# Kernel optimization log

Measured on AMD Instinct MI355X. Metric: run time of the kernel, lower is better.

## Reference

```python
import jax, jax.numpy as jnp
import numpy as np

DIM = 256
HEAD_DIM = 64
NH = DIM // HEAD_DIM
PS = 2  # fine patch size
EPS = 1e-5


def _conv(x, w, b, stride, pad):
    y = jax.lax.conv_general_dilated(x, w, (stride, stride), ((pad, pad), (pad, pad)),
                                     dimension_numbers=('NCHW', 'OIHW', 'NCHW'))
    return y + b[None, :, None, None]


def _bn(x, g, b, m, v):
    s = g * jax.lax.rsqrt(v + EPS)
    return x * s[None, :, None, None] + (b - m * s)[None, :, None, None]


def setup_inputs() -> dict:
    key = jax.random.key(0)
    ks = jax.random.split(key, 24)
    C = DIM
    d = {}
    d['x'] = jax.random.normal(ks[0], (8, C, 64, 64), jnp.float32)
    # Downsample conv (C->C, k=4, s=2, p=1), torch OIHW layout
    d['w_down'] = jax.random.normal(ks[1], (C, C, 4, 4), jnp.float32) * 0.02
    d['b_down'] = jax.random.normal(ks[2], (C,), jnp.float32) * 0.02
    # coarse to_qkv Linear(64 -> 192), stored as [in, out]
    d['w_qkv_c'] = jax.random.normal(ks[3], (HEAD_DIM, 3 * HEAD_DIM), jnp.float32) * 0.05
    d['b_qkv_c'] = jax.random.normal(ks[4], (3 * HEAD_DIM,), jnp.float32) * 0.02
    # Upsample ConvTranspose2d (torch [in, out, kH, kW] layout)
    d['w_up'] = jax.random.normal(ks[5], (C, C, 4, 4), jnp.float32) * 0.02
    d['b_up'] = jax.random.normal(ks[6], (C,), jnp.float32) * 0.02
    # fine to_qkv Linear(64 -> 192)
    d['w_qkv_f'] = jax.random.normal(ks[7], (HEAD_DIM, 3 * HEAD_DIM), jnp.float32) * 0.05
    d['b_qkv_f'] = jax.random.normal(ks[8], (3 * HEAD_DIM,), jnp.float32) * 0.02
    # DWConv: depthwise 3x3 (groups=C) -> BN -> relu6 -> pointwise 1x1 -> BN -> relu6
    d['w_dw'] = jax.random.normal(ks[9], (C, 1, 3, 3), jnp.float32) * 0.1
    d['bn_dw_g'] = jax.random.uniform(ks[10], (C,), jnp.float32) * 0.5 + 0.75
    d['bn_dw_b'] = jax.random.normal(ks[11], (C,), jnp.float32) * 0.1
    d['bn_dw_m'] = jax.random.normal(ks[12], (C,), jnp.float32) * 0.1
    d['bn_dw_v'] = jax.random.uniform(ks[13], (C,), jnp.float32) + 0.5
    d['w_pw'] = jax.random.normal(ks[14], (C, C, 1, 1), jnp.float32) * 0.05
    d['bn_pw_g'] = jax.random.uniform(ks[15], (C,), jnp.float32) * 0.5 + 0.75
    d['bn_pw_b'] = jax.random.normal(ks[16], (C,), jnp.float32) * 0.1
    d['bn_pw_m'] = jax.random.normal(ks[17], (C,), jnp.float32) * 0.1
    d['bn_pw_v'] = jax.random.uniform(ks[18], (C,), jnp.float32) + 0.5
    return d


def reference(x, w_down, b_down, w_qkv_c, b_qkv_c, w_up, b_up, w_qkv_f, b_qkv_f,
              w_dw, bn_dw_g, bn_dw_b, bn_dw_m, bn_dw_v,
              w_pw, bn_pw_g, bn_pw_b, bn_pw_m, bn_pw_v):
    B, C, H, W = x.shape
    nh, hd = C // HEAD_DIM, HEAD_DIM
    scale = hd ** -0.5

    # ---- CoarseSelfAttention ----
    xd = _conv(x, w_down, b_down, 2, 1)           # [B,C,h,w]
    h, w = xd.shape[2], xd.shape[3]
    P = h * w
    tok = xd.reshape(B, nh, hd, P).transpose(0, 1, 3, 2)   # [B,nh,P,hd]
    q, k, v = jnp.split(tok @ w_qkv_c + b_qkv_c, 3, axis=-1)
    attn = jax.nn.softmax(jnp.einsum('bhqd,bhkd->bhqk', q, k) * scale, axis=-1)
    coarse_score = attn.sum(axis=-2)               # [B,nh,P]
    kf = max(1, P // 4)
    top_k = jax.lax.top_k(coarse_score, kf)[1]     # [B,nh,kf]
    out = jnp.einsum('bhqk,bhkd->bhqd', attn, v)
    out = out.transpose(0, 1, 3, 2).reshape(B, C, h, w)
    # ConvTranspose2d(k=4,s=2,p=1) as lhs-dilated conv with flipped/transposed kernel
    wt = jnp.flip(w_up, (2, 3)).transpose(1, 0, 2, 3)
    coarse = jax.lax.conv_general_dilated(out, wt, (1, 1), ((2, 2), (2, 2)),
                                          lhs_dilation=(2, 2),
                                          dimension_numbers=('NCHW', 'OIHW', 'NCHW'))
    coarse = coarse + b_up[None, :, None, None]
    # F.interpolate to (H,W) is identity here: upsample exactly restores HxW

    # ---- TopkSelfAttention ----
    ph, pw = H // PS, W // PS                      # ph*pw == P
    xh = coarse.reshape(B, nh, hd, ph, PS, pw, PS)
    patches = xh.transpose(0, 1, 2, 3, 5, 4, 6).reshape(B, nh, hd, ph * pw, PS, PS)
    idx = jnp.broadcast_to(top_k[:, :, None, :, None, None], (B, nh, hd, kf, PS, PS))
    sel = jnp.take_along_axis(patches, idx, axis=3)        # [B,nh,hd,kf,PS,PS]
    tokf = sel.reshape(B, nh, hd, kf, PS * PS).transpose(0, 1, 3, 4, 2)
    tokf = tokf.reshape(B, nh, kf * PS * PS, hd)
    qf, kk, vf = jnp.split(tokf @ w_qkv_f + b_qkv_f, 3, axis=-1)
    attnf = jax.nn.softmax(jnp.einsum('bhqd,bhkd->bhqk', qf, kk) * scale, axis=-1)
    outf = jnp.einsum('bhqk,bhkd->bhqd', attnf, vf)
    outf = outf.reshape(B, nh, kf, PS * PS, hd).transpose(0, 1, 2, 4, 3)
    outf = outf.reshape(B, nh, kf, hd, PS, PS)     # [B,nh,kf,hd,PS,PS]
    # scatter selected patches back into zeros (topk indices are unique per b,h)
    res = jnp.zeros((B, nh, ph * pw, hd, PS, PS), x.dtype)
    bi = jnp.arange(B)[:, None, None]
    hi = jnp.arange(nh)[None, :, None]
    res = res.at[bi, hi, top_k].set(outf)
    res = res.transpose(0, 1, 3, 2, 4, 5).reshape(B, nh, hd, ph, pw, PS, PS)
    region = res.transpose(0, 1, 2, 3, 5, 4, 6).reshape(B, C, H, W)

    y = coarse + region

    # ---- DWConv feed-forward ----
    yd = jax.lax.conv_general_dilated(y, w_dw, (1, 1), ((1, 1), (1, 1)),
                                      feature_group_count=C,
                                      dimension_numbers=('NCHW', 'OIHW', 'NCHW'))
    yd = jnp.clip(_bn(yd, bn_dw_g, bn_dw_b, bn_dw_m, bn_dw_v), 0.0, 6.0)
    yp = jax.lax.conv_general_dilated(yd, w_pw, (1, 1), ((0, 0), (0, 0)),
                                      dimension_numbers=('NCHW', 'OIHW', 'NCHW'))
    yp = jnp.clip(_bn(yp, bn_pw_g, bn_pw_b, bn_pw_m, bn_pw_v), 0.0, 6.0)
    return yp
```

## Files before the change

kernel.cpp:

```cpp
#include <hip/hip_runtime.h>
#include <cstdint>
#include <cstddef>


#define EPS_ 1e-5f

typedef short bf16x8_t __attribute__((ext_vector_type(8)));
typedef float f32x4_t __attribute__((ext_vector_type(4)));
#define MFMA16(a, b, c) __builtin_amdgcn_mfma_f32_16x16x32_bf16(a, b, c, 0, 0, 0)

__device__ __forceinline__ void cvt1(float f, unsigned short& h, unsigned short& l) {
  unsigned u = __float_as_uint(f);
  unsigned r = u + 0x7FFFu + ((u >> 16) & 1u);
  h = (unsigned short)(r >> 16);
  float lo = f - __uint_as_float(r & 0xFFFF0000u);
  l = (unsigned short)(__float_as_uint(lo) >> 16);
}
__device__ __forceinline__ unsigned cvtpack(float f) {
  unsigned short h, l;
  cvt1(f, h, l);
  return (unsigned)h | ((unsigned)l << 16);
}
__device__ __forceinline__ void cvt2(float f0, float f1, unsigned& hpack, unsigned& lpack) {
  unsigned u0 = __float_as_uint(f0), u1 = __float_as_uint(f1);
  unsigned r0 = u0 + 0x7FFFu + ((u0 >> 16) & 1u);
  unsigned r1 = u1 + 0x7FFFu + ((u1 >> 16) & 1u);
  hpack = (r0 >> 16) | (r1 & 0xFFFF0000u);
  float l0 = f0 - __uint_as_float(r0 & 0xFFFF0000u);
  float l1 = f1 - __uint_as_float(r1 & 0xFFFF0000u);
  lpack = (__float_as_uint(l0) >> 16) | (__float_as_uint(l1) & 0xFFFF0000u);
}
__device__ __forceinline__ unsigned pk_h(unsigned a, unsigned b) {
  return (a & 0xFFFFu) | (b << 16);
}
__device__ __forceinline__ unsigned pk_l(unsigned a, unsigned b) {
  return (a >> 16) | (b & 0xFFFF0000u);
}

__global__ __launch_bounds__(256) void k_pad_x(
    const float* __restrict__ x, unsigned* __restrict__ xphl) {
  const int plane = blockIdx.x;
  const float* src = x + (size_t)plane * 4096;
  unsigned* dst = xphl + (size_t)plane * 4488;
  for (int e = threadIdx.x; e < 4356; e += 256) {
    int r = e / 66, cc = e - r * 66;
    float v = 0.f;
    if (r >= 1 && r <= 64 && cc >= 1 && cc <= 64) v = src[(r - 1) * 64 + (cc - 1)];
    dst[r * 68 + cc] = cvtpack(v);
  }
}

__global__ __launch_bounds__(256) void k_cvt_wdown(
    const float* __restrict__ w, unsigned short* __restrict__ wh,
    unsigned short* __restrict__ wl) {
  int e = blockIdx.x * 256 + threadIdx.x;
  cvt1(w[e], wh[e], wl[e]);
}

__global__ __launch_bounds__(256) void k_cvt_wqkv(
    const float* __restrict__ wq, unsigned short* __restrict__ wh,
    unsigned short* __restrict__ wl) {
  int e = blockIdx.x * 256 + threadIdx.x;
  int col = e >> 6, d = e & 63;
  float f = wq[d * 192 + col];
  if (col < 64) f *= 0.125f;
  cvt1(f, wh[e], wl[e]);
}

__global__ __launch_bounds__(256) void k_cvt_wup(
    const float* __restrict__ w_up, unsigned short* __restrict__ wth,
    unsigned short* __restrict__ wtl) {
  int e = blockIdx.x * 256 + threadIdx.x;
  int kp = e & 1023, oc = (e >> 10) & 255, c = e >> 18;
  int tap = kp >> 8, ic = kp & 255;
  int tk = tap >> 1, txi = tap & 1;
  int ry = c >> 1, rx = c & 1;
  int ky = (1 - ry) + 2 * tk, kx = (1 - rx) + 2 * txi;
  cvt1(w_up[((size_t)(ic * 256 + oc) * 4 + ky) * 4 + kx], wth[e], wtl[e]);
}

__global__ __launch_bounds__(256) void k_cvt_wpw(
    const float* __restrict__ w, unsigned short* __restrict__ wh,
    unsigned short* __restrict__ wl) {
  int e = blockIdx.x * 256 + threadIdx.x;
  cvt1(w[e], wh[e], wl[e]);
}

__device__ __forceinline__ void mfma_chunk(
    const unsigned short (*Ah)[72], const unsigned short (*Al)[72],
    const unsigned short (*Bh)[72], const unsigned short (*Bl)[72],
    f32x4_t (&acc)[4], int wm, int lane) {
  const int l16 = lane & 15, quad = lane >> 4;
#pragma unroll
  for (int ks = 0; ks < 2; ++ks) {
    int ko = ks * 32 + quad * 8;
    bf16x8_t ah = *(const bf16x8_t*)&Ah[wm + l16][ko];
    bf16x8_t al = *(const bf16x8_t*)&Al[wm + l16][ko];
#pragma unroll
    for (int nt = 0; nt < 4; ++nt) {
      bf16x8_t bh = *(const bf16x8_t*)&Bh[nt * 16 + l16][ko];
      bf16x8_t bl = *(const bf16x8_t*)&Bl[nt * 16 + l16][ko];
      acc[nt] = MFMA16(ah, bh, acc[nt]);
      acc[nt] = MFMA16(ah, bl, acc[nt]);
      acc[nt] = MFMA16(al, bh, acc[nt]);
    }
  }
}

__global__ __launch_bounds__(256) void k_conv_down_mfma(
    const unsigned* __restrict__ xphl, const unsigned short* __restrict__ wdh,
    const unsigned short* __restrict__ wdl, const float* __restrict__ bias,
    unsigned* __restrict__ xdhl) {
  __shared__ unsigned short Ah[64][72], Al[64][72], Bh[64][72], Bl[64][72];
  const int t = threadIdx.x;
  const int pix0 = blockIdx.x * 64, oc0 = blockIdx.y * 64;
  const int bimg = pix0 >> 10, pos = pix0 & 1023;
  const int pl = t & 63, icg = t >> 6;
  const int rem = (pix0 + pl) & 1023;
  const int oy = rem >> 5, ox = rem & 31;
  const unsigned* xb = xphl + ((size_t)bimg * 256 + icg) * 4488 + (oy * 2) * 68 + ox * 2;
  const int wave = t >> 6, lane = t & 63, l16 = lane & 15, quad = lane >> 4;
  const int ar = t >> 3, akc = (t & 7) * 8;
  f32x4_t acc[4] = {};
  for (int kb = 0; kb < 4096; kb += 64) {
    bf16x8_t a0h = *(const bf16x8_t*)(wdh + (size_t)(oc0 + ar) * 4096 + kb + akc);
    bf16x8_t a0l = *(const bf16x8_t*)(wdl + (size_t)(oc0 + ar) * 4096 + kb + akc);
    bf16x8_t a1h = *(const bf16x8_t*)(wdh + (size_t)(oc0 + 32 + ar) * 4096 + kb + akc);
    bf16x8_t a1l = *(const bf16x8_t*)(wdl + (size_t)(oc0 + 32 + ar) * 4096 + kb + akc);
    unsigned hA[8], lA[8];
#pragma unroll
    for (int r = 0; r < 4; ++r) {
      uint2 u01 = *(const uint2*)(xb + r * 68);
      uint2 u23 = *(const uint2*)(xb + r * 68 + 2);
      hA[2 * r] = pk_h(u01.x, u01.y); hA[2 * r + 1] = pk_h(u23.x, u23.y);
      lA[2 * r] = pk_l(u01.x, u01.y); lA[2 * r + 1] = pk_l(u23.x, u23.y);
    }
    __syncthreads();
    *(bf16x8_t*)&Ah[ar][akc] = a0h;      *(bf16x8_t*)&Al[ar][akc] = a0l;
    *(bf16x8_t*)&Ah[ar + 32][akc] = a1h; *(bf16x8_t*)&Al[ar + 32][akc] = a1l;
    *(uint4*)&Bh[pl][icg * 16] = make_uint4(hA[0], hA[1], hA[2], hA[3]);
    *(uint4*)&Bh[pl][icg * 16 + 8] = make_uint4(hA[4], hA[5], hA[6], hA[7]);
    *(uint4*)&Bl[pl][icg * 16] = make_uint4(lA[0], lA[1], lA[2], lA[3]);
    *(uint4*)&Bl[pl][icg * 16 + 8] = make_uint4(lA[4], lA[5], lA[6], lA[7]);
    __syncthreads();
    mfma_chunk(Ah, Al, Bh, Bl, acc, wave * 16, lane);
    xb += 4 * 4488;
  }
#pragma unroll
  for (int r = 0; r < 4; ++r) {
    int oc = oc0 + wave * 16 + quad * 4 + r;
    float bv = bias[oc];
#pragma unroll
    for (int nt = 0; nt < 4; ++nt)
      xdhl[((size_t)(bimg * 256 + oc)) * 1024 + pos + nt * 16 + l16] =
          cvtpack(acc[nt][r] + bv);
  }
}

template <int MODE>
__global__ __launch_bounds__(256) void k_qkv_mfma(
    const unsigned* __restrict__ srcp, const float* __restrict__ srcf,
    const unsigned short* __restrict__ wh, const unsigned short* __restrict__ wl,
    const float* __restrict__ bq, const int* __restrict__ topk,
    unsigned short* __restrict__ qh, unsigned short* __restrict__ ql,
    unsigned short* __restrict__ kh, unsigned short* __restrict__ kl,
    unsigned short* __restrict__ vth, unsigned short* __restrict__ vtl) {
  __shared__ unsigned short Ah[64][72], Al[64][72];
  const int t = threadIdx.x;
  const int tok0 = blockIdx.x * 64;
  const int pair = blockIdx.y;
  const int b = pair >> 2, h = pair & 3;
  const int tokl = t & 63, dg = t >> 6;
  unsigned hp[8], lp[8];
  if (MODE == 0) {
    const unsigned* base = srcp + ((size_t)(b * 256 + h * 64 + dg * 16)) * 1024 + tok0 + tokl;
    unsigned u[16];
#pragma unroll
    for (int j = 0; j < 16; ++j) u[j] = base[(size_t)j * 1024];
#pragma unroll
    for (int j = 0; j < 8; ++j) {
      hp[j] = pk_h(u[2 * j], u[2 * j + 1]);
      lp[j] = pk_l(u[2 * j], u[2 * j + 1]);
    }
  } else {
    int tok = tok0 + tokl;
    int pp = topk[pair * 256 + (tok >> 2)];
    int py = (tok >> 1) & 1, px = tok & 1;
    int ry = (pp >> 5) * 2 + py, rx = (pp & 31) * 2 + px;
    const float* base = srcf + ((size_t)(b * 256 + h * 64 + dg * 16)) * 4096 + ry * 64 + rx;
    float fv[16];
#pragma unroll
    for (int j = 0; j < 16; ++j) fv[j] = base[(size_t)j * 4096];
#pragma unroll
    for (int j = 0; j < 8; ++j) cvt2(fv[2 * j], fv[2 * j + 1], hp[j], lp[j]);
  }
  *(uint4*)&Ah[tokl][dg * 16] = make_uint4(hp[0], hp[1], hp[2], hp[3]);
  *(uint4*)&Ah[tokl][dg * 16 + 8] = make_uint4(hp[4], hp[5], hp[6], hp[7]);
  *(uint4*)&Al[tokl][dg * 16] = make_uint4(lp[0], lp[1], lp[2], lp[3]);
  *(uint4*)&Al[tokl][dg * 16 + 8] = make_uint4(lp[4], lp[5], lp[6], lp[7]);
  __syncthreads();
  const int wave = t >> 6, lane = t & 63, l16 = lane & 15, quad = lane >> 4;
  f32x4_t acc[4][3] = {};
#pragma unroll
  for (int ks = 0; ks < 2; ++ks) {
    int ko = ks * 32 + quad * 8;
    bf16x8_t bh0[3], bl0[3];
#pragma unroll
    for (int nt = 0; nt < 3; ++nt) {
      int col = wave * 48 + nt * 16 + l16;
      bh0[nt] = *(const bf16x8_t*)(wh + col * 64 + ko);
      bl0[nt] = *(const bf16x8_t*)(wl + col * 64 + ko);
    }
#pragma unroll
    for (int mt = 0; mt < 4; ++mt) {
      bf16x8_t ah = *(const bf16x8_t*)&Ah[mt * 16 + l16][ko];
      bf16x8_t al = *(const bf16x8_t*)&Al[mt * 16 + l16][ko];
#pragma unroll
      for (int nt = 0; nt < 3; ++nt) {
        acc[mt][nt] = MFMA16(ah, bh0[nt], acc[mt][nt]);
        acc[mt][nt] = MFMA16(ah, bl0[nt], acc[mt][nt]);
        acc[mt][nt] = MFMA16(al, bh0[nt], acc[mt][nt]);
      }
    }
  }
#pragma unroll
  for (int nt = 0; nt < 3; ++nt) {
    int col = wave * 48 + nt * 16 + l16;
    float bqv = bq[col];
    if (col < 64) bqv *= 0.125f;
#pragma unroll
    for (int mt = 0; mt < 4; ++mt) {
#pragma unroll
      for (int r = 0; r < 4; ++r) {
        int tok = tok0 + mt * 16 + quad * 4 + r;
        float val = acc[mt][nt][r] + bqv;
        unsigned short hh, ll;
        cvt1(val, hh, ll);
        if (col < 64) {
          size_t o = ((size_t)pair * 1024 + tok) * 64 + col;
          qh[o] = hh; ql[o] = ll;
        } else if (col < 128) {
          size_t o = ((size_t)pair * 1024 + tok) * 64 + (col - 64);
          kh[o] = hh; kl[o] = ll;
        } else {
          size_t o = ((size_t)pair * 64 + (col - 128)) * 1024 + tok;
          vth[o] = hh; vtl[o] = ll;
        }
      }
    }
  }
}

template <int COARSE>
__global__ __launch_bounds__(256) void k_attn(
    const unsigned short* __restrict__ qh, const unsigned short* __restrict__ ql,
    const unsigned short* __restrict__ kh, const unsigned short* __restrict__ kl,
    const unsigned short* __restrict__ vth, const unsigned short* __restrict__ vtl,
    float* __restrict__ score, unsigned* __restrict__ outc,
    float* __restrict__ outf) {
  __shared__ __align__(16) unsigned short Qb[2][64][72];
  __shared__ __align__(16) unsigned short Kb[2][64][72];
  __shared__ __align__(16) unsigned short Pb[2][64][72];
  __shared__ float mlW[4][2][64];
  __shared__ float mC[64], lC[64];
  __shared__ float colsum[1024];
  const int t = threadIdx.x;
  const int q0 = blockIdx.x * 64;
  const int pair = blockIdx.y;
  const int wave = t >> 6, lane = t & 63;
  const int l16 = lane & 15, quad = lane >> 4;
  const int wm = wave * 16;
  const int sr = t >> 3, skc = (t & 7) * 8;

  const size_t qbase = ((size_t)pair * 1024 + q0) * 64;
#pragma unroll
  for (int i = 0; i < 2; ++i) {
    int r = sr + i * 32;
    *(bf16x8_t*)&Qb[0][r][skc] = *(const bf16x8_t*)(qh + qbase + (size_t)r * 64 + skc);
    *(bf16x8_t*)&Qb[1][r][skc] = *(const bf16x8_t*)(ql + qbase + (size_t)r * 64 + skc);
  }
  if (COARSE) {
#pragma unroll
    for (int i = 0; i < 4; ++i) colsum[t + i * 256] = 0.f;
  }

  const size_t kmbase = (size_t)pair * 1024 * 64;
  const size_t vbase = (size_t)pair * 64 * 1024;

  float mrun[4] = {-1e30f, -1e30f, -1e30f, -1e30f};
  float lrun[4] = {0.f, 0.f, 0.f, 0.f};
  for (int kb = 0; kb < 1024; kb += 64) {
    __syncthreads();
#pragma unroll
    for (int i = 0; i < 2; ++i) {
      int r = sr + i * 32;
      *(bf16x8_t*)&Kb[0][r][skc] = *(const bf16x8_t*)(kh + kmbase + (size_t)(kb + r) * 64 + skc);
      *(bf16x8_t*)&Kb[1][r][skc] = *(const bf16x8_t*)(kl + kmbase + (size_t)(kb + r) * 64 + skc);
    }
    __syncthreads();
    f32x4_t acc[4] = {};
    mfma_chunk(Kb[0], Kb[1], Qb[0], Qb[1], acc, wm, lane);
#pragma unroll
    for (int nt = 0; nt < 4; ++nt) {
      float m0 = fmaxf(fmaxf(acc[nt][0], acc[nt][1]), fmaxf(acc[nt][2], acc[nt][3]));
      m0 = fmaxf(m0, __shfl_xor(m0, 16));
      m0 = fmaxf(m0, __shfl_xor(m0, 32));
      float mn = fmaxf(mrun[nt], m0);
      float s0 = __expf(acc[nt][0] - mn) + __expf(acc[nt][1] - mn) +
                 __expf(acc[nt][2] - mn) + __expf(acc[nt][3] - mn);
      s0 += __shfl_xor(s0, 16);
      s0 += __shfl_xor(s0, 32);
      lrun[nt] = lrun[nt] * __expf(mrun[nt] - mn) + s0;
      mrun[nt] = mn;
    }
  }
  __syncthreads();
  if (quad == 0) {
#pragma unroll
    for (int nt = 0; nt < 4; ++nt) {
      mlW[wave][0][nt * 16 + l16] = mrun[nt];
      mlW[wave][1][nt * 16 + l16] = lrun[nt];
    }
  }
  __syncthreads();
  if (t < 64) {
    float m0 = mlW[0][0][t], m1 = mlW[1][0][t], m2 = mlW[2][0][t], m3 = mlW[3][0][t];
    float mm = fmaxf(fmaxf(m0, m1), fmaxf(m2, m3));
    float ll = mlW[0][1][t] * __expf(m0 - mm) + mlW[1][1][t] * __expf(m1 - mm) +
               mlW[2][1][t] * __expf(m2 - mm) + mlW[3][1][t] * __expf(m3 - mm);
    mC[t] = mm;
    lC[t] = 1.0f / ll;
  }
  __syncthreads();
  float mq[4], il[4];
#pragma unroll
  for (int nt = 0; nt < 4; ++nt) {
    mq[nt] = mC[nt * 16 + l16];
    il[nt] = lC[nt * 16 + l16];
  }

  f32x4_t accO[4] = {};
  for (int kb = 0; kb < 1024; kb += 64) {
    __syncthreads();
#pragma unroll
    for (int i = 0; i < 2; ++i) {
      int r = sr + i * 32;
      *(bf16x8_t*)&Kb[0][r][skc] = *(const bf16x8_t*)(kh + kmbase + (size_t)(kb + r) * 64 + skc);
      *(bf16x8_t*)&Kb[1][r][skc] = *(const bf16x8_t*)(kl + kmbase + (size_t)(kb + r) * 64 + skc);
    }
    __syncthreads();
    f32x4_t acc[4] = {};
    mfma_chunk(Kb[0], Kb[1], Qb[0], Qb[1], acc, wm, lane);
    float P[4][4];
#pragma unroll
    for (int nt = 0; nt < 4; ++nt)
#pragma unroll
      for (int r = 0; r < 4; ++r) P[nt][r] = __expf(acc[nt][r] - mq[nt]) * il[nt];
    if (COARSE) {
#pragma unroll
      for (int r = 0; r < 4; ++r) {
        float cs = P[0][r] + P[1][r] + P[2][r] + P[3][r];
        cs += __shfl_xor(cs, 1);
        cs += __shfl_xor(cs, 2);
        cs += __shfl_xor(cs, 4);
        cs += __shfl_xor(cs, 8);
        if (l16 == 0) colsum[kb + wm + quad * 4 + r] += cs;
      }
    }
    __syncthreads();
#pragma unroll
    for (int nt = 0; nt < 4; ++nt) {
      unsigned h01, l01, h23, l23;
      cvt2(P[nt][0], P[nt][1], h01, l01);
      cvt2(P[nt][2], P[nt][3], h23, l23);
      *(uint2*)&Pb[0][nt * 16 + l16][wm + quad * 4] = make_uint2(h01, h23);
      *(uint2*)&Pb[1][nt * 16 + l16][wm + quad * 4] = make_uint2(l01, l23);
    }
#pragma unroll
    for (int i = 0; i < 2; ++i) {
      int r = sr + i * 32;
      *(bf16x8_t*)&Kb[0][r][skc] = *(const bf16x8_t*)(vth + vbase + (size_t)r * 1024 + kb + skc);
      *(bf16x8_t*)&Kb[1][r][skc] = *(const bf16x8_t*)(vtl + vbase + (size_t)r * 1024 + kb + skc);
    }
    __syncthreads();
    mfma_chunk(Pb[0], Pb[1], Kb[0], Kb[1], accO, wm, lane);
  }
  __syncthreads();

  if (COARSE) {
#pragma unroll
    for (int i = 0; i < 4; ++i)
      atomicAdd(&score[pair * 1024 + t + i * 256], colsum[t + i * 256]);
    float (*Tr)[68] = reinterpret_cast<float(*)[68]>(&Pb[0][0][0]);
#pragma unroll
    for (int nt = 0; nt < 4; ++nt)
#pragma unroll
      for (int r = 0; r < 4; ++r)
        Tr[nt * 16 + l16][wm + quad * 4 + r] = accO[nt][r];
    __syncthreads();
    const int b = pair >> 2, h = pair & 3;
#pragma unroll
    for (int i = 0; i < 16; ++i) {
      int e = t + i * 256;
      int d = e >> 6, ql_ = e & 63;
      int pix = q0 + ql_;
      int iy = (pix >> 5) + 1, ix = (pix & 31) + 1;
      outc[((size_t)(b * 256 + h * 64 + d)) * 1156 + iy * 34 + ix] = cvtpack(Tr[d][ql_]);
    }
  } else {
#pragma unroll
    for (int nt = 0; nt < 4; ++nt)
#pragma unroll
      for (int r = 0; r < 4; ++r) {
        int qm = q0 + wm + quad * 4 + r;
        outf[((size_t)pair * 1024 + qm) * 64 + nt * 16 + l16] = accO[nt][r];
      }
  }
}

__global__ __launch_bounds__(256) void k_topk(
    const float* __restrict__ score, int* __restrict__ idx) {
  __shared__ unsigned long long key[1024];
  const int pair = blockIdx.x;
  const int t = threadIdx.x;
#pragma unroll
  for (int j = 0; j < 4; ++j) {
    int i = t + j * 256;
    unsigned u = __float_as_uint(score[pair * 1024 + i]);
    u = u ^ ((u & 0x80000000u) ? 0xFFFFFFFFu : 0x80000000u);
    u = ~u;
    key[i] = ((unsigned long long)u << 32) | (unsigned)i;
  }
  __syncthreads();
  for (int k = 2; k <= 1024; k <<= 1) {
    for (int j = k >> 1; j > 0; j >>= 1) {
      for (int w = 0; w < 4; ++w) {
        int i = t + w * 256;
        int l = i ^ j;
        if (l > i) {
          bool up = ((i & k) == 0);
          unsigned long long a = key[i], b = key[l];
          if ((a > b) == up) { key[i] = b; key[l] = a; }
        }
      }
      __syncthreads();
    }
  }
  idx[pair * 256 + t] = (int)(key[t] & 0xFFFFFFFFu);
}

__global__ __launch_bounds__(256) void k_convT_mfma(
    const unsigned* __restrict__ inp, const unsigned short* __restrict__ wth,
    const unsigned short* __restrict__ wtl, const float* __restrict__ bias,
    float* __restrict__ out) {
  __shared__ unsigned short Ah[64][72], Al[64][72], Bh[64][72], Bl[64][72];
  const int t = threadIdx.x;
  const int pix0 = blockIdx.x * 64;
  const int oc0 = blockIdx.y * 64;
  const int cls = blockIdx.z;
  const int ry = cls >> 1, rx = cls & 1;
  const int b = pix0 >> 10;
  const int wave = t >> 6, lane = t & 63;
  const int l16 = lane & 15, quad = lane >> 4;
  const int pixl = t & 63, icg = t >> 6;
  const int remg = (pix0 + pixl) & 1023;
  const int tyy = remg >> 5, txx = remg & 31;
  f32x4_t acc[4] = {};
  const size_t wbase = ((size_t)cls * 256 + oc0) * 1024;
  for (int kb = 0; kb < 1024; kb += 64) {
    const int tap = kb >> 8, ic0 = kb & 255;
    const int tk = tap >> 1, txi = tap & 1;
    const int iy = tyy + ry + 1 - tk, ix = txx + rx + 1 - txi;
    const unsigned* p = inp + (size_t)(b * 256 + ic0 + icg * 16) * 1156 + iy * 34 + ix;
    unsigned u[16];
#pragma unroll
    for (int j = 0; j < 16; ++j) u[j] = p[(size_t)j * 1156];
    unsigned hp[8], lpk[8];
#pragma unroll
    for (int j = 0; j < 8; ++j) {
      hp[j] = pk_h(u[2 * j], u[2 * j + 1]);
      lpk[j] = pk_l(u[2 * j], u[2 * j + 1]);
    }
    bf16x8_t a0h, a0l, a1h, a1l;
    {
      int r = t >> 3, kc = (t & 7) * 8;
      a0h = *(const bf16x8_t*)(wth + wbase + (size_t)r * 1024 + kb + kc);
      a0l = *(const bf16x8_t*)(wtl + wbase + (size_t)r * 1024 + kb + kc);
      a1h = *(const bf16x8_t*)(wth + wbase + (size_t)(r + 32) * 1024 + kb + kc);
      a1l = *(const bf16x8_t*)(wtl + wbase + (size_t)(r + 32) * 1024 + kb + kc);
    }
    __syncthreads();
    {
      int r = t >> 3, kc = (t & 7) * 8;
      *(bf16x8_t*)&Ah[r][kc] = a0h;      *(bf16x8_t*)&Al[r][kc] = a0l;
      *(bf16x8_t*)&Ah[r + 32][kc] = a1h; *(bf16x8_t*)&Al[r + 32][kc] = a1l;
    }
    *(uint4*)&Bh[pixl][icg * 16] = make_uint4(hp[0], hp[1], hp[2], hp[3]);
    *(uint4*)&Bh[pixl][icg * 16 + 8] = make_uint4(hp[4], hp[5], hp[6], hp[7]);
    *(uint4*)&Bl[pixl][icg * 16] = make_uint4(lpk[0], lpk[1], lpk[2], lpk[3]);
    *(uint4*)&Bl[pixl][icg * 16 + 8] = make_uint4(lpk[4], lpk[5], lpk[6], lpk[7]);
    __syncthreads();
    mfma_chunk(Ah, Al, Bh, Bl, acc, wave * 16, lane);
  }
  __syncthreads();
#pragma unroll
  for (int r = 0; r < 4; ++r) {
    int oc = oc0 + wave * 16 + quad * 4 + r;
    float bvs = bias[oc];
#pragma unroll
    for (int nt = 0; nt < 4; ++nt) {
      int pix = pix0 + nt * 16 + l16;
      int rem2 = pix & 1023;
      int y = (rem2 >> 5) * 2 + ry, xx = (rem2 & 31) * 2 + rx;
      out[((size_t)(b * 256 + oc) * 64 + y) * 64 + xx] = acc[nt][r] + bvs;
    }
  }
}

__global__ __launch_bounds__(256) void k_scatter(
    const float* __restrict__ outf, const int* __restrict__ idx,
    float* __restrict__ y) {
  int g = blockIdx.x * 256 + threadIdx.x;
  int pair = g >> 16;
  int rem = g & 65535;
  int tok = rem >> 6, d = rem & 63;
  int b = pair >> 2, h = pair & 3;
  int pp = idx[pair * 256 + (tok >> 2)];
  int py = (tok >> 1) & 1, px = tok & 1;
  int ry = (pp >> 5) * 2 + py, rx = (pp & 31) * 2 + px;
  y[((size_t)(b * 256 + h * 64 + d) * 64 + ry) * 64 + rx] += outf[g];
}

__global__ __launch_bounds__(256) void k_dwconv(
    const float* __restrict__ y, const float* __restrict__ wdw,
    const float* __restrict__ g, const float* __restrict__ bb,
    const float* __restrict__ m, const float* __restrict__ vv,
    unsigned* __restrict__ ydhl) {
  int gi = blockIdx.x * 256 + threadIdx.x;
  int x = gi & 63, yy = (gi >> 6) & 63, ch = (gi >> 12) & 255, b = gi >> 20;
  const float* plane = y + (size_t)(b * 256 + ch) * 4096;
  const float* wc = wdw + ch * 9;
  float s = 0.f;
#pragma unroll
  for (int ky = 0; ky < 3; ++ky) {
    int iy = yy + ky - 1;
    if (iy < 0 || iy >= 64) continue;
#pragma unroll
    for (int kx = 0; kx < 3; ++kx) {
      int ix = x + kx - 1;
      if (ix < 0 || ix >= 64) continue;
      s = fmaf(plane[iy * 64 + ix], wc[ky * 3 + kx], s);
    }
  }
  float sc = g[ch] * rsqrtf(vv[ch] + EPS_);
  float val = s * sc + (bb[ch] - m[ch] * sc);
  ydhl[gi] = cvtpack(fminf(fmaxf(val, 0.f), 6.f));
}

__global__ __launch_bounds__(256) void k_pw_mfma(
    const unsigned* __restrict__ ydhl, const unsigned short* __restrict__ wh,
    const unsigned short* __restrict__ wl, const float* __restrict__ g,
    const float* __restrict__ bb, const float* __restrict__ m,
    const float* __restrict__ vv, float* __restrict__ out) {
  __shared__ unsigned short Ah[64][72], Al[64][72], Bh[64][72], Bl[64][72];
  const int t = threadIdx.x;
  const int pix0 = blockIdx.x * 64;
  const int oc0 = blockIdx.y * 64;
  const int b = pix0 >> 12, pos0 = pix0 & 4095;
  const int wave = t >> 6, lane = t & 63;
  const int l16 = lane & 15, quad = lane >> 4;
  const int pixl = t & 63, icg = t >> 6;
  f32x4_t acc[4] = {};
  for (int kb = 0; kb < 256; kb += 64) {
    unsigned u[16];
#pragma unroll
    for (int j = 0; j < 16; ++j)
      u[j] = ydhl[(size_t)(b * 256 + kb + icg * 16 + j) * 4096 + pos0 + pixl];
    unsigned hp[8], lpk[8];
#pragma unroll
    for (int j = 0; j < 8; ++j) {
      hp[j] = pk_h(u[2 * j], u[2 * j + 1]);
      lpk[j] = pk_l(u[2 * j], u[2 * j + 1]);
    }
    bf16x8_t a0h, a0l, a1h, a1l;
    {
      int r = t >> 3, kc = (t & 7) * 8;
      a0h = *(const bf16x8_t*)(wh + (size_t)(oc0 + r) * 256 + kb + kc);
      a0l = *(const bf16x8_t*)(wl + (size_t)(oc0 + r) * 256 + kb + kc);
      a1h = *(const bf16x8_t*)(wh + (size_t)(oc0 + r + 32) * 256 + kb + kc);
      a1l = *(const bf16x8_t*)(wl + (size_t)(oc0 + r + 32) * 256 + kb + kc);
    }
    __syncthreads();
    {
      int r = t >> 3, kc = (t & 7) * 8;
      *(bf16x8_t*)&Ah[r][kc] = a0h;      *(bf16x8_t*)&Al[r][kc] = a0l;
      *(bf16x8_t*)&Ah[r + 32][kc] = a1h; *(bf16x8_t*)&Al[r + 32][kc] = a1l;
    }
    *(uint4*)&Bh[pixl][icg * 16] = make_uint4(hp[0], hp[1], hp[2], hp[3]);
    *(uint4*)&Bh[pixl][icg * 16 + 8] = make_uint4(hp[4], hp[5], hp[6], hp[7]);
    *(uint4*)&Bl[pixl][icg * 16] = make_uint4(lpk[0], lpk[1], lpk[2], lpk[3]);
    *(uint4*)&Bl[pixl][icg * 16 + 8] = make_uint4(lpk[4], lpk[5], lpk[6], lpk[7]);
    __syncthreads();
    mfma_chunk(Ah, Al, Bh, Bl, acc, wave * 16, lane);
    __syncthreads();
  }
#pragma unroll
  for (int r = 0; r < 4; ++r) {
    int oc = oc0 + wave * 16 + quad * 4 + r;
    float sc = g[oc] * rsqrtf(vv[oc] + EPS_);
    float off = bb[oc] - m[oc] * sc;
#pragma unroll
    for (int nt = 0; nt < 4; ++nt) {
      int pix = pos0 + nt * 16 + l16;
      float val = fminf(fmaxf(acc[nt][r] * sc + off, 0.f), 6.f);
      out[(size_t)(b * 256 + oc) * 4096 + pix] = val;
    }
  }
}

extern "C" void kernel_launch(void* const* d_in, const int* in_sizes, int n_in,
                              void* d_out, int out_size, void* d_ws, size_t ws_size,
                              hipStream_t stream) {
  (void)in_sizes; (void)n_in; (void)out_size; (void)ws_size;
  const float* x       = (const float*)d_in[0];
  const float* w_down  = (const float*)d_in[1];
  const float* b_down  = (const float*)d_in[2];
  const float* w_qkv_c = (const float*)d_in[3];
  const float* b_qkv_c = (const float*)d_in[4];
  const float* w_up    = (const float*)d_in[5];
  const float* b_up    = (const float*)d_in[6];
  const float* w_qkv_f = (const float*)d_in[7];
  const float* b_qkv_f = (const float*)d_in[8];
  const float* w_dw    = (const float*)d_in[9];
  const float* bn_dw_g = (const float*)d_in[10];
  const float* bn_dw_b = (const float*)d_in[11];
  const float* bn_dw_m = (const float*)d_in[12];
  const float* bn_dw_v = (const float*)d_in[13];
  const float* w_pw    = (const float*)d_in[14];
  const float* bn_pw_g = (const float*)d_in[15];
  const float* bn_pw_b = (const float*)d_in[16];
  const float* bn_pw_m = (const float*)d_in[17];
  const float* bn_pw_v = (const float*)d_in[18];

  float* ws = (float*)d_ws;
  unsigned*       xphl   = (unsigned*)ws;
  unsigned*       ydhl   = (unsigned*)ws;
  unsigned short* qh     = (unsigned short*)(ws + 33554432);
  unsigned short* ql     = (unsigned short*)(ws + 34603008);
  unsigned short* kh     = (unsigned short*)(ws + 35651584);
  unsigned short* kl     = (unsigned short*)(ws + 36700160);
  unsigned short* vth    = (unsigned short*)(ws + 37748736);
  unsigned short* vtl    = (unsigned short*)(ws + 38797312);
  unsigned*       xdhl   = (unsigned*)(ws + 39845888);
  unsigned*       outcphl= (unsigned*)(ws + 41943040);
  float*          coarse = ws + 44310528;
  float*          outf   = ws + 52699136;
  float*          score  = ws + 54796288;
  unsigned short* wdh    = (unsigned short*)(ws + 54829056);
  unsigned short* wdl    = (unsigned short*)(ws + 55353344);
  unsigned short* wt_hi  = (unsigned short*)(ws + 55877632);
  unsigned short* wt_lo  = (unsigned short*)(ws + 56401920);
  unsigned short* wpw_hi = (unsigned short*)(ws + 56926208);
  unsigned short* wpw_lo = (unsigned short*)(ws + 56958976);
  unsigned short* wqh_c  = (unsigned short*)(ws + 56991744);
  unsigned short* wql_c  = (unsigned short*)(ws + 56997888);
  unsigned short* wqh_f  = (unsigned short*)(ws + 57004032);
  unsigned short* wql_f  = (unsigned short*)(ws + 57010176);
  int*            idx    = (int*)(ws + 57016320);

  hipMemsetAsync(score, 0, 32768 * sizeof(float), stream);
  hipMemsetAsync(outcphl, 0, (size_t)2367488 * sizeof(unsigned), stream);
  k_pad_x<<<2048, 256, 0, stream>>>(x, xphl);
  k_cvt_wdown<<<4096, 256, 0, stream>>>(w_down, wdh, wdl);
  k_cvt_wqkv<<<48, 256, 0, stream>>>(w_qkv_c, wqh_c, wql_c);
  k_cvt_wqkv<<<48, 256, 0, stream>>>(w_qkv_f, wqh_f, wql_f);
  k_cvt_wup<<<4096, 256, 0, stream>>>(w_up, wt_hi, wt_lo);
  k_cvt_wpw<<<256, 256, 0, stream>>>(w_pw, wpw_hi, wpw_lo);

  k_conv_down_mfma<<<dim3(128, 4), 256, 0, stream>>>(xphl, wdh, wdl, b_down, xdhl);
  k_qkv_mfma<0><<<dim3(16, 32), 256, 0, stream>>>(xdhl, nullptr, wqh_c, wql_c, b_qkv_c,
                                                  nullptr, qh, ql, kh, kl, vth, vtl);
  k_attn<1><<<dim3(16, 32), 256, 0, stream>>>(qh, ql, kh, kl, vth, vtl, score,
                                              outcphl, nullptr);
  k_topk<<<32, 256, 0, stream>>>(score, idx);
  k_convT_mfma<<<dim3(128, 4, 4), 256, 0, stream>>>(outcphl, wt_hi, wt_lo, b_up, coarse);

  k_qkv_mfma<1><<<dim3(16, 32), 256, 0, stream>>>(nullptr, coarse, wqh_f, wql_f, b_qkv_f,
                                                  idx, qh, ql, kh, kl, vth, vtl);
  k_attn<0><<<dim3(16, 32), 256, 0, stream>>>(qh, ql, kh, kl, vth, vtl, nullptr,
                                              nullptr, outf);
  k_scatter<<<8192, 256, 0, stream>>>(outf, idx, coarse);
  k_dwconv<<<32768, 256, 0, stream>>>(coarse, w_dw, bn_dw_g, bn_dw_b, bn_dw_m, bn_dw_v, ydhl);
  k_pw_mfma<<<dim3(512, 4), 256, 0, stream>>>(ydhl, wpw_hi, wpw_lo, bn_pw_g, bn_pw_b,
                                              bn_pw_m, bn_pw_v, (float*)d_out);
}
```

Before: 627.4 us.

## Use 2D wave tiling in conv GEMMs and enlarge pixel tiles to 128

Each wave in the MFMA conv kernels now computes a 2D sub-tile (32x32 or 32x64) instead of a 16-row strip across all columns. This lets A fragments be reused across several B tiles and cuts LDS fragment reads per MFMA. ConvT and pointwise kernels also double the pixel tile to 128 per block, halving grid size and weight reloads. The costs are more LDS and registers per block and fewer blocks, which may lower occupancy. The convT and pointwise kernels also drop a trailing barrier.

```diff
diff --git a/kernel.cpp b/kernel.cpp
--- a/kernel.cpp
+++ b/kernel.cpp
@@ -103,6 +103,62 @@
       acc[nt] = MFMA16(ah, bh, acc[nt]);
       acc[nt] = MFMA16(ah, bl, acc[nt]);
       acc[nt] = MFMA16(al, bh, acc[nt]);
+    }
+  }
+}
+
+__device__ __forceinline__ void mfma_tile2x2(
+    const unsigned short (*Ah)[72], const unsigned short (*Al)[72],
+    const unsigned short (*Bh)[72], const unsigned short (*Bl)[72],
+    f32x4_t (&acc)[2][2], int wm, int wn, int lane) {
+  const int l16 = lane & 15, quad = lane >> 4;
+#pragma unroll
+  for (int ks = 0; ks < 2; ++ks) {
+    int ko = ks * 32 + quad * 8;
+    bf16x8_t ah[2], al[2];
+#pragma unroll
+    for (int mt = 0; mt < 2; ++mt) {
+      ah[mt] = *(const bf16x8_t*)&Ah[wm + mt * 16 + l16][ko];
+      al[mt] = *(const bf16x8_t*)&Al[wm + mt * 16 + l16][ko];
+    }
+#pragma unroll
+    for (int nt = 0; nt < 2; ++nt) {
+      bf16x8_t bh = *(const bf16x8_t*)&Bh[wn + nt * 16 + l16][ko];
+      bf16x8_t bl = *(const bf16x8_t*)&Bl[wn + nt * 16 + l16][ko];
+#pragma unroll
+      for (int mt = 0; mt < 2; ++mt) {
+        acc[mt][nt] = MFMA16(ah[mt], bh, acc[mt][nt]);
+        acc[mt][nt] = MFMA16(ah[mt], bl, acc[mt][nt]);
+        acc[mt][nt] = MFMA16(al[mt], bh, acc[mt][nt]);
+      }
+    }
+  }
+}
+
+__device__ __forceinline__ void mfma_tile2x4(
+    const unsigned short (*Ah)[72], const unsigned short (*Al)[72],
+    const unsigned short (*Bh)[72], const unsigned short (*Bl)[72],
+    f32x4_t (&acc)[2][4], int wm, int wn, int lane) {
+  const int l16 = lane & 15, quad = lane >> 4;
+#pragma unroll
+  for (int ks = 0; ks < 2; ++ks) {
+    int ko = ks * 32 + quad * 8;
+    bf16x8_t ah[2], al[2];
+#pragma unroll
+    for (int mt = 0; mt < 2; ++mt) {
+      ah[mt] = *(const bf16x8_t*)&Ah[wm + mt * 16 + l16][ko];
+      al[mt] = *(const bf16x8_t*)&Al[wm + mt * 16 + l16][ko];
+    }
+#pragma unroll
+    for (int nt = 0; nt < 4; ++nt) {
+      bf16x8_t bh = *(const bf16x8_t*)&Bh[wn + nt * 16 + l16][ko];
+      bf16x8_t bl = *(const bf16x8_t*)&Bl[wn + nt * 16 + l16][ko];
+#pragma unroll
+      for (int mt = 0; mt < 2; ++mt) {
+        acc[mt][nt] = MFMA16(ah[mt], bh, acc[mt][nt]);
+        acc[mt][nt] = MFMA16(ah[mt], bl, acc[mt][nt]);
+        acc[mt][nt] = MFMA16(al[mt], bh, acc[mt][nt]);
+      }
     }
   }
 }
@@ -120,41 +176,54 @@
   const int oy = rem >> 5, ox = rem & 31;
   const unsigned* xb = xphl + ((size_t)bimg * 256 + icg) * 4488 + (oy * 2) * 68 + ox * 2;
   const int wave = t >> 6, lane = t & 63, l16 = lane & 15, quad = lane >> 4;
-  const int ar = t >> 3, akc = (t & 7) * 8;
-  f32x4_t acc[4] = {};
+  const int wm = (wave & 1) * 32, wn = (wave >> 1) * 32;
+  const int ar = t >> 2, ac = (t & 3) * 16;
+  const unsigned short* wra = wdh + (size_t)(oc0 + ar) * 4096 + ac;
+  const unsigned short* wrl = wdl + (size_t)(oc0 + ar) * 4096 + ac;
+  f32x4_t acc[2][2] = {};
   for (int kb = 0; kb < 4096; kb += 64) {
-    bf16x8_t a0h = *(const bf16x8_t*)(wdh + (size_t)(oc0 + ar) * 4096 + kb + akc);
-    bf16x8_t a0l = *(const bf16x8_t*)(wdl + (size_t)(oc0 + ar) * 4096 + kb + akc);
-    bf16x8_t a1h = *(const bf16x8_t*)(wdh + (size_t)(oc0 + 32 + ar) * 4096 + kb + akc);
-    bf16x8_t a1l = *(const bf16x8_t*)(wdl + (size_t)(oc0 + 32 + ar) * 4096 + kb + akc);
-    unsigned hA[8], lA[8];
+    bf16x8_t a0 = *(const bf16x8_t*)(wra + kb);
+    bf16x8_t a1 = *(const bf16x8_t*)(wra + kb + 8);
+    bf16x8_t a2 = *(const bf16x8_t*)(wrl + kb);
+    bf16x8_t a3 = *(const bf16x8_t*)(wrl + kb + 8);
+    unsigned u[16];
 #pragma unroll
     for (int r = 0; r < 4; ++r) {
       uint2 u01 = *(const uint2*)(xb + r * 68);
       uint2 u23 = *(const uint2*)(xb + r * 68 + 2);
-      hA[2 * r] = pk_h(u01.x, u01.y); hA[2 * r + 1] = pk_h(u23.x, u23.y);
-      lA[2 * r] = pk_l(u01.x, u01.y); lA[2 * r + 1] = pk_l(u23.x, u23.y);
-    }
-    __syncthreads();
-    *(bf16x8_t*)&Ah[ar][akc] = a0h;      *(bf16x8_t*)&Al[ar][akc] = a0l;
-    *(bf16x8_t*)&Ah[ar + 32][akc] = a1h; *(bf16x8_t*)&Al[ar + 32][akc] = a1l;
-    *(uint4*)&Bh[pl][icg * 16] = make_uint4(hA[0], hA[1], hA[2], hA[3]);
-    *(uint4*)&Bh[pl][icg * 16 + 8] = make_uint4(hA[4], hA[5], hA[6], hA[7]);
-    *(uint4*)&Bl[pl][icg * 16] = make_uint4(lA[0], lA[1], lA[2], lA[3]);
-    *(uint4*)&Bl[pl][icg * 16 + 8] = make_uint4(lA[4], lA[5], lA[6], lA[7]);
-    __syncthreads();
-    mfma_chunk(Ah, Al, Bh, Bl, acc, wave * 16, lane);
+      u[4 * r + 0] = u01.x; u[4 * r + 1] = u01.y;
+      u[4 * r + 2] = u23.x; u[4 * r + 3] = u23.y;
+    }
+    unsigned hp[8], lp[8];
+#pragma unroll
+    for (int j = 0; j < 8; ++j) {
+      hp[j] = pk_h(u[2 * j], u[2 * j + 1]);
+      lp[j] = pk_l(u[2 * j], u[2 * j + 1]);
+    }
+    __syncthreads();
+    *(bf16x8_t*)&Ah[ar][ac] = a0;
+    *(bf16x8_t*)&Ah[ar][ac + 8] = a1;
+    *(bf16x8_t*)&Al[ar][ac] = a2;
+    *(bf16x8_t*)&Al[ar][ac + 8] = a3;
+    *(uint4*)&Bh[pl][icg * 16] = make_uint4(hp[0], hp[1], hp[2], hp[3]);
+    *(uint4*)&Bh[pl][icg * 16 + 8] = make_uint4(hp[4], hp[5], hp[6], hp[7]);
+    *(uint4*)&Bl[pl][icg * 16] = make_uint4(lp[0], lp[1], lp[2], lp[3]);
+    *(uint4*)&Bl[pl][icg * 16 + 8] = make_uint4(lp[4], lp[5], lp[6], lp[7]);
+    __syncthreads();
+    mfma_tile2x2(Ah, Al, Bh, Bl, acc, wm, wn, lane);
     xb += 4 * 4488;
   }
 #pragma unroll
-  for (int r = 0; r < 4; ++r) {
-    int oc = oc0 + wave * 16 + quad * 4 + r;
-    float bv = bias[oc];
-#pragma unroll
-    for (int nt = 0; nt < 4; ++nt)
-      xdhl[((size_t)(bimg * 256 + oc)) * 1024 + pos + nt * 16 + l16] =
-          cvtpack(acc[nt][r] + bv);
-  }
+  for (int mt = 0; mt < 2; ++mt)
+#pragma unroll
+    for (int r = 0; r < 4; ++r) {
+      int oc = oc0 + wm + mt * 16 + quad * 4 + r;
+      float bv = bias[oc];
+#pragma unroll
+      for (int nt = 0; nt < 2; ++nt)
+        xdhl[((size_t)(bimg * 256 + oc)) * 1024 + pos + wn + nt * 16 + l16] =
+            cvtpack(acc[mt][nt][r] + bv);
+    }
 }
 
 template <int MODE>
@@ -453,68 +522,74 @@
     const unsigned* __restrict__ inp, const unsigned short* __restrict__ wth,
     const unsigned short* __restrict__ wtl, const float* __restrict__ bias,
     float* __restrict__ out) {
-  __shared__ unsigned short Ah[64][72], Al[64][72], Bh[64][72], Bl[64][72];
+  __shared__ unsigned short Ah[64][72], Al[64][72];
+  __shared__ unsigned short Bh[128][72], Bl[128][72];
   const int t = threadIdx.x;
-  const int pix0 = blockIdx.x * 64;
+  const int pix0 = blockIdx.x * 128;
   const int oc0 = blockIdx.y * 64;
   const int cls = blockIdx.z;
   const int ry = cls >> 1, rx = cls & 1;
   const int b = pix0 >> 10;
   const int wave = t >> 6, lane = t & 63;
   const int l16 = lane & 15, quad = lane >> 4;
-  const int pixl = t & 63, icg = t >> 6;
-  const int remg = (pix0 + pixl) & 1023;
+  const int wm = (wave & 1) * 32, wn = (wave >> 1) * 64;
+  const int pl = t & 127, icg = t >> 7;
+  const int remg = (pix0 + pl) & 1023;
   const int tyy = remg >> 5, txx = remg & 31;
-  f32x4_t acc[4] = {};
-  const size_t wbase = ((size_t)cls * 256 + oc0) * 1024;
+  const int ar = t >> 2, ac = (t & 3) * 16;
+  const size_t wbase = ((size_t)cls * 256 + oc0 + ar) * 1024 + ac;
+  f32x4_t acc[2][4] = {};
   for (int kb = 0; kb < 1024; kb += 64) {
     const int tap = kb >> 8, ic0 = kb & 255;
     const int tk = tap >> 1, txi = tap & 1;
     const int iy = tyy + ry + 1 - tk, ix = txx + rx + 1 - txi;
-    const unsigned* p = inp + (size_t)(b * 256 + ic0 + icg * 16) * 1156 + iy * 34 + ix;
-    unsigned u[16];
-#pragma unroll
-    for (int j = 0; j < 16; ++j) u[j] = p[(size_t)j * 1156];
-    unsigned hp[8], lpk[8];
-#pragma unroll
-    for (int j = 0; j < 8; ++j) {
+    const unsigned* p = inp + (size_t)(b * 256 + ic0 + icg * 32) * 1156 + iy * 34 + ix;
+    unsigned u[32];
+#pragma unroll
+    for (int j = 0; j < 32; ++j) u[j] = p[(size_t)j * 1156];
+    unsigned hp[16], lpk[16];
+#pragma unroll
+    for (int j = 0; j < 16; ++j) {
       hp[j] = pk_h(u[2 * j], u[2 * j + 1]);
       lpk[j] = pk_l(u[2 * j], u[2 * j + 1]);
     }
-    bf16x8_t a0h, a0l, a1h, a1l;
+    bf16x8_t a0 = *(const bf16x8_t*)(wth + wbase + kb);
+    bf16x8_t a1 = *(const bf16x8_t*)(wth + wbase + kb + 8);
+    bf16x8_t a2 = *(const bf16x8_t*)(wtl + wbase + kb);
+    bf16x8_t a3 = *(const bf16x8_t*)(wtl + wbase + kb + 8);
+    __syncthreads();
+    *(bf16x8_t*)&Ah[ar][ac] = a0;
+    *(bf16x8_t*)&Ah[ar][ac + 8] = a1;
+    *(bf16x8_t*)&Al[ar][ac] = a2;
+    *(bf16x8_t*)&Al[ar][ac + 8] = a3;
     {
-      int r = t >> 3, kc = (t & 7) * 8;
-      a0h = *(const bf16x8_t*)(wth + wbase + (size_t)r * 1024 + kb + kc);
-      a0l = *(const bf16x8_t*)(wtl + wbase + (size_t)r * 1024 + kb + kc);
-      a1h = *(const bf16x8_t*)(wth + wbase + (size_t)(r + 32) * 1024 + kb + kc);
-      a1l = *(const bf16x8_t*)(wtl + wbase + (size_t)(r + 32) * 1024 + kb + kc);
-    }
-    __syncthreads();
-    {
-      int r = t >> 3, kc = (t & 7) * 8;
-      *(bf16x8_t*)&Ah[r][kc] = a0h;      *(bf16x8_t*)&Al[r][kc] = a0l;
-      *(bf16x8_t*)&Ah[r + 32][kc] = a1h; *(bf16x8_t*)&Al[r + 32][kc] = a1l;
-    }
-    *(uint4*)&Bh[pixl][icg * 16] = make_uint4(hp[0], hp[1], hp[2], hp[3]);
-    *(uint4*)&Bh[pixl][icg * 16 + 8] = make_uint4(hp[4], hp[5], hp[6], hp[7]);
-    *(uint4*)&Bl[pixl][icg * 16] = make_uint4(lpk[0], lpk[1], lpk[2], lpk[3]);
-    *(uint4*)&Bl[pixl][icg * 16 + 8] = make_uint4(lpk[4], lpk[5], lpk[6], lpk[7]);
-    __syncthreads();
-    mfma_chunk(Ah, Al, Bh, Bl, acc, wave * 16, lane);
-  }
-  __syncthreads();
-#pragma unroll
-  for (int r = 0; r < 4; ++r) {
-    int oc = oc0 + wave * 16 + quad * 4 + r;
-    float bvs = bias[oc];
-#pragma unroll
-    for (int nt = 0; nt < 4; ++nt) {
-      int pix = pix0 + nt * 16 + l16;
-      int rem2 = pix & 1023;
-      int y = (rem2 >> 5) * 2 + ry, xx = (rem2 & 31) * 2 + rx;
-      out[((size_t)(b * 256 + oc) * 64 + y) * 64 + xx] = acc[nt][r] + bvs;
-    }
-  }
+      int kc = icg * 32;
+      *(uint4*)&Bh[pl][kc] = make_uint4(hp[0], hp[1], hp[2], hp[3]);
+      *(uint4*)&Bh[pl][kc + 8] = make_uint4(hp[4], hp[5], hp[6], hp[7]);
+      *(uint4*)&Bh[pl][kc + 16] = make_uint4(hp[8], hp[9], hp[10], hp[11]);
+      *(uint4*)&Bh[pl][kc + 24] = make_uint4(hp[12], hp[13], hp[14], hp[15]);
+      *(uint4*)&Bl[pl][kc] = make_uint4(lpk[0], lpk[1], lpk[2], lpk[3]);
+      *(uint4*)&Bl[pl][kc + 8] = make_uint4(lpk[4], lpk[5], lpk[6], lpk[7]);
+      *(uint4*)&Bl[pl][kc + 16] = make_uint4(lpk[8], lpk[9], lpk[10], lpk[11]);
+      *(uint4*)&Bl[pl][kc + 24] = make_uint4(lpk[12], lpk[13], lpk[14], lpk[15]);
+    }
+    __syncthreads();
+    mfma_tile2x4(Ah, Al, Bh, Bl, acc, wm, wn, lane);
+  }
+#pragma unroll
+  for (int mt = 0; mt < 2; ++mt)
+#pragma unroll
+    for (int r = 0; r < 4; ++r) {
+      int oc = oc0 + wm + mt * 16 + quad * 4 + r;
+      float bvs = bias[oc];
+#pragma unroll
+      for (int nt = 0; nt < 4; ++nt) {
+        int pix = pix0 + wn + nt * 16 + l16;
+        int rem2 = pix & 1023;
+        int y = (rem2 >> 5) * 2 + ry, xx = (rem2 & 31) * 2 + rx;
+        out[((size_t)(b * 256 + oc) * 64 + y) * 64 + xx] = acc[mt][nt][r] + bvs;
+      }
+    }
 }
 
 __global__ __launch_bounds__(256) void k_scatter(
@@ -562,60 +637,66 @@
     const unsigned short* __restrict__ wl, const float* __restrict__ g,
     const float* __restrict__ bb, const float* __restrict__ m,
     const float* __restrict__ vv, float* __restrict__ out) {
-  __shared__ unsigned short Ah[64][72], Al[64][72], Bh[64][72], Bl[64][72];
+  __shared__ unsigned short Ah[64][72], Al[64][72];
+  __shared__ unsigned short Bh[128][72], Bl[128][72];
   const int t = threadIdx.x;
-  const int pix0 = blockIdx.x * 64;
+  const int pix0 = blockIdx.x * 128;
   const int oc0 = blockIdx.y * 64;
   const int b = pix0 >> 12, pos0 = pix0 & 4095;
   const int wave = t >> 6, lane = t & 63;
   const int l16 = lane & 15, quad = lane >> 4;
-  const int pixl = t & 63, icg = t >> 6;
-  f32x4_t acc[4] = {};
+  const int wm = (wave & 1) * 32, wn = (wave >> 1) * 64;
+  const int pl = t & 127, icg = t >> 7;
+  const int ar = t >> 2, ac = (t & 3) * 16;
+  f32x4_t acc[2][4] = {};
   for (int kb = 0; kb < 256; kb += 64) {
-    unsigned u[16];
-#pragma unroll
-    for (int j = 0; j < 16; ++j)
-      u[j] = ydhl[(size_t)(b * 256 + kb + icg * 16 + j) * 4096 + pos0 + pixl];
-    unsigned hp[8], lpk[8];
-#pragma unroll
-    for (int j = 0; j < 8; ++j) {
+    const unsigned* p = ydhl + (size_t)(b * 256 + kb + icg * 32) * 4096 + pos0 + pl;
+    unsigned u[32];
+#pragma unroll
+    for (int j = 0; j < 32; ++j) u[j] = p[(size_t)j * 4096];
+    unsigned hp[16], lpk[16];
+#pragma unroll
+    for (int j = 0; j < 16; ++j) {
       hp[j] = pk_h(u[2 * j], u[2 * j + 1]);
       lpk[j] = pk_l(u[2 * j], u[2 * j + 1]);
     }
-    bf16x8_t a0h, a0l, a1h, a1l;
+    bf16x8_t a0 = *(const bf16x8_t*)(wh + (size_t)(oc0 + ar) * 256 + kb + ac);
+    bf16x8_t a1 = *(const bf16x8_t*)(wh + (size_t)(oc0 + ar) * 256 + kb + ac + 8);
+    bf16x8_t a2 = *(const bf16x8_t*)(wl + (size_t)(oc0 + ar) * 256 + kb + ac);
+    bf16x8_t a3 = *(const bf16x8_t*)(wl + (size_t)(oc0 + ar) * 256 + kb + ac + 8);
+    __syncthreads();
+    *(bf16x8_t*)&Ah[ar][ac] = a0;
+    *(bf16x8_t*)&Ah[ar][ac + 8] = a1;
+    *(bf16x8_t*)&Al[ar][ac] = a2;
+    *(bf16x8_t*)&Al[ar][ac + 8] = a3;
     {
-      int r = t >> 3, kc = (t & 7) * 8;
-      a0h = *(const bf16x8_t*)(wh + (size_t)(oc0 + r) * 256 + kb + kc);
-      a0l = *(const bf16x8_t*)(wl + (size_t)(oc0 + r) * 256 + kb + kc);
-      a1h = *(const bf16x8_t*)(wh + (size_t)(oc0 + r + 32) * 256 + kb + kc);
-      a1l = *(const bf16x8_t*)(wl + (size_t)(oc0 + r + 32) * 256 + kb + kc);
-    }
-    __syncthreads();
-    {
-      int r = t >> 3, kc = (t & 7) * 8;
-      *(bf16x8_t*)&Ah[r][kc] = a0h;      *(bf16x8_t*)&Al[r][kc] = a0l;
-      *(bf16x8_t*)&Ah[r + 32][kc] = a1h; *(bf16x8_t*)&Al[r + 32][kc] = a1l;
-    }
-    *(uint4*)&Bh[pixl][icg * 16] = make_uint4(hp[0], hp[1], hp[2], hp[3]);
-    *(uint4*)&Bh[pixl][icg * 16 + 8] = make_uint4(hp[4], hp[5], hp[6], hp[7]);
-    *(uint4*)&Bl[pixl][icg * 16] = make_uint4(lpk[0], lpk[1], lpk[2], lpk[3]);
-    *(uint4*)&Bl[pixl][icg * 16 + 8] = make_uint4(lpk[4], lpk[5], lpk[6], lpk[7]);
-    __syncthreads();
-    mfma_chunk(Ah, Al, Bh, Bl, acc, wave * 16, lane);
-    __syncthreads();
-  }
-#pragma unroll
-  for (int r = 0; r < 4; ++r) {
-    int oc = oc0 + wave * 16 + quad * 4 + r;
-    float sc = g[oc] * rsqrtf(vv[oc] + EPS_);
-    float off = bb[oc] - m[oc] * sc;
-#pragma unroll
-    for (int nt = 0; nt < 4; ++nt) {
-      int pix = pos0 + nt * 16 + l16;
-      float val = fminf(fmaxf(acc[nt][r] * sc + off, 0.f), 6.f);
-      out[(size_t)(b * 256 + oc) * 4096 + pix] = val;
-    }
-  }
+      int kc = icg * 32;
+      *(uint4*)&Bh[pl][kc] = make_uint4(hp[0], hp[1], hp[2], hp[3]);
+      *(uint4*)&Bh[pl][kc + 8] = make_uint4(hp[4], hp[5], hp[6], hp[7]);
+      *(uint4*)&Bh[pl][kc + 16] = make_uint4(hp[8], hp[9], hp[10], hp[11]);
+      *(uint4*)&Bh[pl][kc + 24] = make_uint4(hp[12], hp[13], hp[14], hp[15]);
+      *(uint4*)&Bl[pl][kc] = make_uint4(lpk[0], lpk[1], lpk[2], lpk[3]);
+      *(uint4*)&Bl[pl][kc + 8] = make_uint4(lpk[4], lpk[5], lpk[6], lpk[7]);
+      *(uint4*)&Bl[pl][kc + 16] = make_uint4(lpk[8], lpk[9], lpk[10], lpk[11]);
+      *(uint4*)&Bl[pl][kc + 24] = make_uint4(lpk[12], lpk[13], lpk[14], lpk[15]);
+    }
+    __syncthreads();
+    mfma_tile2x4(Ah, Al, Bh, Bl, acc, wm, wn, lane);
+  }
+#pragma unroll
+  for (int mt = 0; mt < 2; ++mt)
+#pragma unroll
+    for (int r = 0; r < 4; ++r) {
+      int oc = oc0 + wm + mt * 16 + quad * 4 + r;
+      float sc = g[oc] * rsqrtf(vv[oc] + EPS_);
+      float off = bb[oc] - m[oc] * sc;
+#pragma unroll
+      for (int nt = 0; nt < 4; ++nt) {
+        int pix = pos0 + wn + nt * 16 + l16;
+        float val = fminf(fmaxf(acc[mt][nt][r] * sc + off, 0.f), 6.f);
+        out[(size_t)(b * 256 + oc) * 4096 + pix] = val;
+      }
+    }
 }
 
 extern "C" void kernel_launch(void* const* d_in, const int* in_sizes, int n_in,
@@ -683,7 +764,7 @@
   k_attn<1><<<dim3(16, 32), 256, 0, stream>>>(qh, ql, kh, kl, vth, vtl, score,
                                               outcphl, nullptr);
   k_topk<<<32, 256, 0, stream>>>(score, idx);
-  k_convT_mfma<<<dim3(128, 4, 4), 256, 0, stream>>>(outcphl, wt_hi, wt_lo, b_up, coarse);
+  k_convT_mfma<<<dim3(64, 4, 4), 256, 0, stream>>>(outcphl, wt_hi, wt_lo, b_up, coarse);
 
   k_qkv_mfma<1><<<dim3(16, 32), 256, 0, stream>>>(nullptr, coarse, wqh_f, wql_f, b_qkv_f,
                                                   idx, qh, ql, kh, kl, vth, vtl);
@@ -691,6 +772,6 @@
                                               nullptr, outf);
   k_scatter<<<8192, 256, 0, stream>>>(outf, idx, coarse);
   k_dwconv<<<32768, 256, 0, stream>>>(coarse, w_dw, bn_dw_g, bn_dw_b, bn_dw_m, bn_dw_v, ydhl);
-  k_pw_mfma<<<dim3(512, 4), 256, 0, stream>>>(ydhl, wpw_hi, wpw_lo, bn_pw_g, bn_pw_b,
+  k_pw_mfma<<<dim3(256, 4), 256, 0, stream>>>(ydhl, wpw_hi, wpw_lo, bn_pw_g, bn_pw_b,
                                               bn_pw_m, bn_pw_v, (float*)d_out);
 }
```

Measured after the change: 617.0 us. Within noise of the previous version (-1.7%).
